# Kernel optimization log

Hardware: AMD Instinct MI355X
Metric: run time of the kernel (lower is better)

## Reference

```python
import jax, jax.numpy as jnp
import numpy as np

NUM_HEADS = 8
EPS = 1e-12  # torch F.normalize default eps


def conv1x1(x, w):
    # x: [b,c,h,w], w: [o,c]
    return jnp.einsum('bchw,oc->bohw', x, w)


def dwconv3x3(x, w):
    # depthwise 3x3, w: [c,1,3,3]
    return jax.lax.conv_general_dilated(
        x, w, window_strides=(1, 1), padding=((1, 1), (1, 1)),
        dimension_numbers=('NCHW', 'OIHW', 'NCHW'),
        feature_group_count=x.shape[1])


def l2norm(x):
    n = jnp.sqrt(jnp.sum(x * x, axis=-1, keepdims=True))
    return x / jnp.maximum(n, EPS)


def channel_attn(q, k, v, temperature, b, c, h, w):
    hd = c // NUM_HEADS
    q = l2norm(q.reshape(b, NUM_HEADS, hd, h * w))
    k = l2norm(k.reshape(b, NUM_HEADS, hd, h * w))
    v = v.reshape(b, NUM_HEADS, hd, h * w)
    attn = jnp.einsum('bndl,bnel->bnde', q, k) * temperature  # [b,nh,hd,hd]
    attn = jax.nn.softmax(attn, axis=-1)
    out = jnp.einsum('bnde,bnel->bndl', attn, v)
    return out.reshape(b, c, h, w)


def fdfp(x, w1, w2, h, w):
    xf = jnp.fft.rfft2(x, norm='ortho')  # over last two axes
    xfreq = jnp.concatenate([xf.real, xf.imag], axis=1)
    xfreq = conv1x1(xfreq, w1)
    xfreq = jax.nn.gelu(xfreq, approximate=False)
    xfreq = conv1x1(xfreq, w2)
    c2 = xfreq.shape[1] // 2
    xc = jax.lax.complex(xfreq[:, :c2], xfreq[:, c2:])
    return jnp.fft.irfft2(xc, s=(h, w), norm='ortho')


def setup_inputs() -> dict:
    key = jax.random.key(0)
    ks = jax.random.split(key, 10)
    dim = 192
    b, h, w = 4, 128, 128
    s = 0.05
    return {
        'x': jax.random.normal(ks[0], (b, dim, h, w), jnp.float32),
        'w_qkv1': jax.random.normal(ks[1], (3 * dim, dim), jnp.float32) * s,
        'w_qkv1_dw': jax.random.normal(ks[2], (3 * dim, 1, 3, 3), jnp.float32) * s,
        'w_proj1': jax.random.normal(ks[3], (dim, dim), jnp.float32) * s,
        'w_fdfp1': jax.random.normal(ks[4], (2 * dim, 2 * dim), jnp.float32) * s,
        'w_fdfp2': jax.random.normal(ks[5], (2 * dim, 2 * dim), jnp.float32) * s,
        'w_kv2': jax.random.normal(ks[6], (2 * dim, dim), jnp.float32) * s,
        'w_kv2_dw': jax.random.normal(ks[7], (2 * dim, 1, 3, 3), jnp.float32) * s,
        'w_proj2': jax.random.normal(ks[8], (dim, dim), jnp.float32) * s,
        'temperature': jnp.ones((NUM_HEADS, 1, 1), jnp.float32),
    }


def reference(x, w_qkv1, w_qkv1_dw, w_proj1, w_fdfp1, w_fdfp2,
              w_kv2, w_kv2_dw, w_proj2, temperature):
    b, c, h, w = x.shape
    # Stage 1: spatial-domain transposed (channel) attention
    qkv1 = dwconv3x3(conv1x1(x, w_qkv1), w_qkv1_dw)
    q1, k1, v1 = jnp.split(qkv1, 3, axis=1)
    out1 = channel_attn(q1, k1, v1, temperature, b, c, h, w)
    out1 = conv1x1(out1, w_proj1)
    # Stage 2: frequency-domain query, spatial K/V from stage-1 output
    q2 = fdfp(x, w_fdfp1, w_fdfp2, h, w)
    kv2 = dwconv3x3(conv1x1(out1, w_kv2), w_kv2_dw)
    k2, v2 = jnp.split(kv2, 2, axis=1)
    out2 = channel_attn(q2, k2, v2, temperature, b, c, h, w)
    out2 = conv1x1(out2, w_proj2)
    return out2
```

## Files before the change

kernel.cpp:

```cpp
#include <hip/hip_runtime.h>
#include <math.h>

typedef _Float16 half_t;
typedef half_t h8v __attribute__((ext_vector_type(8)));
typedef half_t h4v __attribute__((ext_vector_type(4)));
typedef float f32x4 __attribute__((ext_vector_type(4)));

namespace {
constexpr int DIMC = 192;
constexpr int NB = 4;
constexpr int HH = 128, WW = 128;
constexpr int HW = HH * WW;
constexpr int NH = 8, HD = 24;
constexpr int FP = 80;
constexpr long LT_PART = 128L * 192 * FP;
constexpr long LT_B    = 2 * LT_PART;
constexpr long LT_ROW  = 192L * FP;
constexpr long XB  = 192L * HW;
constexpr long CB0 = 0;
constexpr long CB1 = 15728640;
constexpr long OFF_T1 = 37748736;
constexpr long OFF_Q2 = 50331648;
constexpr long OFF_S  = 62914560;
constexpr long OFF_KT = 0;
constexpr long OFF_KF = 25165824;
constexpr long OFF_O2 = 0;
constexpr int  GSL = 64;
constexpr long SM_INVQ1 = OFF_S;
constexpr long SM_INVK1 = OFF_S + 768;
constexpr long SM_INVQ2 = OFF_S + 1536;
constexpr long SM_INVK2 = OFF_S + 2304;
constexpr long SM_ATT   = OFF_S + 3072;
constexpr long H0       = OFF_S + 168960;
constexpr long H_WQKV = H0;
constexpr long H_WF   = H0 + 55296;
constexpr long H_W1   = H0 + 92160;
constexpr long H_W2   = H0 + 165888;
constexpr long H_PRJ  = H0 + 239616;
constexpr long H_B2   = H0 + 258048;
constexpr long H_B3   = H0 + 290816;
constexpr long H_B1T  = H0 + 323584;
constexpr long H_B4T  = H0 + 333824;
constexpr float PI2 = 6.283185307179586476f;
}

__global__ void cvt16_k(const float* __restrict__ in, half_t* __restrict__ o, int n) {
    int i = blockIdx.x * 256 + threadIdx.x;
    if (i < n) o[i] = (half_t)in[i];
}
__global__ void initB1t_k(half_t* __restrict__ B) {
    int idx = blockIdx.x * 256 + threadIdx.x;
    if (idx >= 160 * 128) return;
    int j = idx / 128, k = idx % 128;
    float v = 0.f;
    if (j < 65) v = cosf(PI2 * ((k * j) & 127) / 128.f) * (1.f / 128.f);
    else if (j >= 80 && j < 145) v = -sinf(PI2 * ((k * (j - 80)) & 127) / 128.f) * (1.f / 128.f);
    B[idx] = (half_t)v;
}
__global__ void initB2h_k(half_t* __restrict__ B) {
    int idx = blockIdx.x * 256 + threadIdx.x;
    int m = idx >> 8, cin = idx & 255;
    int pd = m >> 7, ky = m & 127;
    int ps = cin >> 7, y = cin & 127;
    float c, s; sincosf(PI2 * ((ky * y) & 127) / 128.f, &s, &c);
    float v = (pd == 0) ? (ps == 0 ? c : s) : (ps == 0 ? -s : c);
    B[idx] = (half_t)v;
}
__global__ void initB3h_k(half_t* __restrict__ B) {
    int idx = blockIdx.x * 256 + threadIdx.x;
    int m = idx >> 8, cin = idx & 255;
    int pd = m >> 7, y = m & 127;
    int ps = cin >> 7, ky = cin & 127;
    float c, s; sincosf(PI2 * ((y * ky) & 127) / 128.f, &s, &c);
    float v = (pd == 0) ? (ps == 0 ? c : -s) : (ps == 0 ? s : c);
    B[idx] = (half_t)v;
}
__global__ void initB4t_k(half_t* __restrict__ B) {
    int idx = blockIdx.x * 256 + threadIdx.x;
    if (idx >= 128 * 160) return;
    int j = idx / 160, k = idx % 160;
    float v = 0.f;
    if (k < 80) {
        if (k == 0) v = 1.f / 128.f;
        else if (k < 64) v = 2.f * cosf(PI2 * ((k * j) & 127) / 128.f) / 128.f;
        else if (k == 64) v = cosf(PI2 * ((64 * j) & 127) / 128.f) / 128.f;
    } else {
        int kx = k - 80;
        if (kx >= 1 && kx < 64) v = -2.f * sinf(PI2 * ((kx * j) & 127) / 128.f) / 128.f;
    }
    B[idx] = (half_t)v;
}
__global__ void fusew_k(const float* __restrict__ wkv, const float* __restrict__ wproj,
                        half_t* __restrict__ wf) {
    int o = blockIdx.x, c = threadIdx.x;
    float acc = 0.f;
    for (int m = 0; m < 192; ++m) acc += wkv[o * 192 + m] * wproj[m * 192 + c];
    wf[o * 192 + c] = (half_t)acc;
}

template<int NW>
__global__ __launch_bounds__(NW * 64) void kcv(
    const half_t* __restrict__ W, const float* __restrict__ X, long xB,
    float* __restrict__ out, long oB) {
    __shared__ __align__(16) half_t S[6 * 64 * 40];
    const int t = threadIdx.x;
    const long p0 = (long)blockIdx.x * 64;
    const long xb = (long)blockIdx.y * xB;
    const long ob = (long)blockIdx.y * oB;
    const int lane = t & 63, wv = t >> 6;
    const int fr = lane & 15, fg = lane >> 4;
    {
        const int sp = t & 63;
        const int g = t >> 6;
        const float* gp = X + xb + p0 + sp;
        for (int grp = g; grp < 48; grp += NW) {
            int ci0 = grp * 4;
            h4v h;
#pragma unroll
            for (int j = 0; j < 4; ++j) h[j] = (half_t)gp[(long)(ci0 + j) * HW];
            *(h4v*)&S[((ci0 >> 5) * 64 + sp) * 40 + (ci0 & 31)] = h;
        }
    }
    __syncthreads();
    f32x4 acc[3][4];
#pragma unroll
    for (int m = 0; m < 3; ++m)
#pragma unroll
        for (int n = 0; n < 4; ++n) acc[m][n] = {0.f, 0.f, 0.f, 0.f};
    for (int k0 = 0; k0 < 192; k0 += 32) {
        const int s = k0 >> 5;
        h8v a[3], bb[4];
#pragma unroll
        for (int m = 0; m < 3; ++m)
            a[m] = *(const h8v*)(W + (long)(wv * 48 + m * 16 + fr) * 192 + k0 + fg * 8);
#pragma unroll
        for (int n = 0; n < 4; ++n)
            bb[n] = *(const h8v*)&S[(s * 64 + n * 16 + fr) * 40 + fg * 8];
#pragma unroll
        for (int m = 0; m < 3; ++m)
#pragma unroll
            for (int n = 0; n < 4; ++n)
                acc[m][n] = __builtin_amdgcn_mfma_f32_16x16x32_f16(a[m], bb[n], acc[m][n], 0, 0, 0);
    }
#pragma unroll
    for (int m = 0; m < 3; ++m)
#pragma unroll
        for (int i = 0; i < 4; ++i) {
            int o = wv * 48 + m * 16 + fg * 4 + i;
            float* row = out + ob + (long)o * HW + p0;
#pragma unroll
            for (int n = 0; n < 4; ++n) row[n * 16 + fr] = acc[m][n][i];
        }
}

template<int IN16, int OUT16>
__global__ __launch_bounds__(256) void k2big(
    const half_t* __restrict__ B16,
    const void* __restrict__ Xv, void* __restrict__ outv) {
    __shared__ __align__(16) half_t Xh[8 * 64 * 40];
    const int t = threadIdx.x;
    const long p0 = (long)blockIdx.x * 64;
    const long xb = (long)blockIdx.y * LT_B;
    const int lane = t & 63, wv = t >> 6;
    const int fr = lane & 15, fg = lane >> 4;
    {
        const int sp = t & 63;
        const int c0 = t >> 6;
#pragma unroll 8
        for (int j = 0; j < 64; ++j) {
            int ci = c0 + j * 4;
            long rb = (ci < 128) ? (long)ci * LT_ROW : (long)(ci - 128) * LT_ROW + LT_PART;
            half_t hv;
            if (IN16) hv = ((const half_t*)Xv)[xb + p0 + sp + rb];
            else      hv = (half_t)((const float*)Xv)[xb + p0 + sp + rb];
            Xh[((ci >> 5) * 64 + sp) * 40 + (ci & 31)] = hv;
        }
    }
    __syncthreads();
    f32x4 acc[4][4];
#pragma unroll
    for (int m = 0; m < 4; ++m)
#pragma unroll
        for (int n = 0; n < 4; ++n) acc[m][n] = {0.f, 0.f, 0.f, 0.f};
    for (int k0 = 0; k0 < 256; k0 += 32) {
        const int s = k0 >> 5;
        h8v a[4], bb[4];
#pragma unroll
        for (int m = 0; m < 4; ++m)
            a[m] = *(const h8v*)(B16 + (long)(wv * 64 + m * 16 + fr) * 256 + k0 + fg * 8);
#pragma unroll
        for (int n = 0; n < 4; ++n)
            bb[n] = *(const h8v*)&Xh[(s * 64 + n * 16 + fr) * 40 + fg * 8];
#pragma unroll
        for (int m = 0; m < 4; ++m)
#pragma unroll
            for (int n = 0; n < 4; ++n)
                acc[m][n] = __builtin_amdgcn_mfma_f32_16x16x32_f16(a[m], bb[n], acc[m][n], 0, 0, 0);
    }
#pragma unroll
    for (int m = 0; m < 4; ++m)
#pragma unroll
        for (int i = 0; i < 4; ++i) {
            int o = wv * 64 + m * 16 + fg * 4 + i;
            long oadr = xb + ((o < 128) ? (long)o * LT_ROW : (long)(o - 128) * LT_ROW + LT_PART);
#pragma unroll
            for (int n = 0; n < 4; ++n) {
                long idx = oadr + p0 + n * 16 + fr;
                if (OUT16) ((half_t*)outv)[idx] = (half_t)acc[m][n][i];
                else       ((float*)outv)[idx]  = acc[m][n][i];
            }
        }
}

__global__ __launch_bounds__(512) void kff4h(
    const half_t* __restrict__ W1, const half_t* __restrict__ W2,
    const half_t* __restrict__ X, half_t* __restrict__ out) {
    __shared__ __align__(16) half_t S[12 * 64 * 40];
    const int t = threadIdx.x;
    const long p0 = (long)blockIdx.x * 64;
    const long xb = (long)blockIdx.y * LT_B;
    const int lane = t & 63, wv = t >> 6;
    const int fr = lane & 15, fg = lane >> 4;
    {
        const int sp = t & 63;
        const int g = t >> 6;
        long pa; { long p = p0 + sp; long q = p / 80; pa = q * LT_ROW + (p - q * 80); }
        const half_t* gp = X + xb + pa;
#pragma unroll
        for (int ch = 0; ch < 12; ++ch) {
            int ci0 = ch * 32 + g * 4;
            h4v h;
#pragma unroll
            for (int j = 0; j < 4; ++j) {
                int ci = ci0 + j;
                long rb = (ci < 192) ? (long)ci * 80 : (long)(ci - 192) * 80 + LT_PART;
                h[j] = gp[rb];
            }
            *(h4v*)&S[(ch * 64 + sp) * 40 + g * 4] = h;
        }
    }
    __syncthreads();
    f32x4 acc[3][4];
#pragma unroll
    for (int m = 0; m < 3; ++m)
#pragma unroll
        for (int n = 0; n < 4; ++n) acc[m][n] = {0.f, 0.f, 0.f, 0.f};
    for (int k0 = 0; k0 < 384; k0 += 32) {
        const int s = k0 >> 5;
        h8v a[3], bb[4];
#pragma unroll
        for (int m = 0; m < 3; ++m)
            a[m] = *(const h8v*)(W1 + (long)(wv * 48 + m * 16 + fr) * 384 + k0 + fg * 8);
#pragma unroll
        for (int n = 0; n < 4; ++n)
            bb[n] = *(const h8v*)&S[(s * 64 + n * 16 + fr) * 40 + fg * 8];
#pragma unroll
        for (int m = 0; m < 3; ++m)
#pragma unroll
            for (int n = 0; n < 4; ++n)
                acc[m][n] = __builtin_amdgcn_mfma_f32_16x16x32_f16(a[m], bb[n], acc[m][n], 0, 0, 0);
    }
    __syncthreads();
#pragma unroll
    for (int m = 0; m < 3; ++m)
#pragma unroll
        for (int n = 0; n < 4; ++n) {
            int o4 = wv * 48 + m * 16 + fg * 4;
            int p = n * 16 + fr;
            h4v h;
#pragma unroll
            for (int i = 0; i < 4; ++i) {
                float v = acc[m][n][i];
                v = 0.5f * v * (1.f + erff(v * 0.70710678118654752f));
                h[i] = (half_t)v;
            }
            *(h4v*)&S[((o4 >> 5) * 64 + p) * 40 + (o4 & 31)] = h;
        }
#pragma unroll
    for (int m = 0; m < 3; ++m)
#pragma unroll
        for (int n = 0; n < 4; ++n) acc[m][n] = {0.f, 0.f, 0.f, 0.f};
    __syncthreads();
    for (int k0 = 0; k0 < 384; k0 += 32) {
        const int s = k0 >> 5;
        h8v a[3], bb[4];
#pragma unroll
        for (int m = 0; m < 3; ++m)
            a[m] = *(const h8v*)(W2 + (long)(wv * 48 + m * 16 + fr) * 384 + k0 + fg * 8);
#pragma unroll
        for (int n = 0; n < 4; ++n)
            bb[n] = *(const h8v*)&S[(s * 64 + n * 16 + fr) * 40 + fg * 8];
#pragma unroll
        for (int m = 0; m < 3; ++m)
#pragma unroll
            for (int n = 0; n < 4; ++n)
                acc[m][n] = __builtin_amdgcn_mfma_f32_16x16x32_f16(a[m], bb[n], acc[m][n], 0, 0, 0);
    }
    long pe[4];
#pragma unroll
    for (int n = 0; n < 4; ++n) {
        long p = p0 + n * 16 + fr;
        long q = p / 80; pe[n] = q * LT_ROW + (p - q * 80);
    }
#pragma unroll
    for (int m = 0; m < 3; ++m)
#pragma unroll
        for (int i = 0; i < 4; ++i) {
            int o = wv * 48 + m * 16 + fg * 4 + i;
            long oadr = xb + ((o < 192) ? (long)o * 80 : (long)(o - 192) * 80 + LT_PART);
#pragma unroll
            for (int n = 0; n < 4; ++n) out[oadr + pe[n]] = (half_t)acc[m][n][i];
        }
}

template<int NF, int NORM, int OUT16>
__global__ __launch_bounds__(256) void k1m(
    const float* __restrict__ A, long aBatch, long aC, long aRow, int aSplit, long aHiOff, int K,
    const uint* __restrict__ Bt32,
    void* __restrict__ outv, long oBatch, long oC, long oRow, int oSplit, long oHiOff,
    float* __restrict__ inv) {
    __shared__ __align__(16) half_t Ah[128 * 40];
    __shared__ __align__(16) half_t Bh[160 * 40];
    const int t = threadIdx.x;
    const long ab = (long)blockIdx.z * aBatch + (long)blockIdx.x * aC;
    const long ob = (long)blockIdx.z * oBatch + (long)blockIdx.x * oC;
    const int N = NF * 32;
    const int lane = t & 63, wv = t >> 6;
    const int wm = wv >> 1, wn = wv & 1;
    const int fr = lane & 15, fg = lane >> 4;
    const int sr = t >> 1, shalf = t & 1;
    const int Kw = K >> 1;
    f32x4 acc[4][NF];
#pragma unroll
    for (int m = 0; m < 4; ++m)
#pragma unroll
        for (int n = 0; n < NF; ++n) acc[m][n] = {0.f, 0.f, 0.f, 0.f};
    for (int k0 = 0; k0 < K; k0 += 32) {
        __syncthreads();
        {
            int cb = k0 + shalf * 16;
            long rb = (cb < aSplit) ? (long)cb : (long)(cb - aSplit) + aHiOff;
            const float* g = A + ab + (long)sr * aRow + rb;
            float4 v0 = *(const float4*)g;
            float4 v1 = *(const float4*)(g + 4);
            float4 v2 = *(const float4*)(g + 8);
            float4 v3 = *(const float4*)(g + 12);
            h8v h0, h1;
            h0[0] = (half_t)v0.x; h0[1] = (half_t)v0.y; h0[2] = (half_t)v0.z; h0[3] = (half_t)v0.w;
            h0[4] = (half_t)v1.x; h0[5] = (half_t)v1.y; h0[6] = (half_t)v1.z; h0[7] = (half_t)v1.w;
            h1[0] = (half_t)v2.x; h1[1] = (half_t)v2.y; h1[2] = (half_t)v2.z; h1[3] = (half_t)v2.w;
            h1[4] = (half_t)v3.x; h1[5] = (half_t)v3.y; h1[6] = (half_t)v3.z; h1[7] = (half_t)v3.w;
            *(h8v*)&Ah[sr * 40 + shalf * 16] = h0;
            *(h8v*)&Ah[sr * 40 + shalf * 16 + 8] = h1;
        }
        for (int j = t; j < N * 16; j += 256) {
            int n = j >> 4, kw = j & 15;
            *(uint*)&Bh[n * 40 + kw * 2] = Bt32[(long)n * Kw + (k0 >> 1) + kw];
        }
        __syncthreads();
        h8v a[4], bb[NF];
#pragma unroll
        for (int m = 0; m < 4; ++m) a[m] = *(const h8v*)&Ah[(wm * 64 + m * 16 + fr) * 40 + fg * 8];
#pragma unroll
        for (int n = 0; n < NF; ++n) bb[n] = *(const h8v*)&Bh[(wn * NF * 16 + n * 16 + fr) * 40 + fg * 8];
#pragma unroll
        for (int m = 0; m < 4; ++m)
#pragma unroll
            for (int n = 0; n < NF; ++n)
                acc[m][n] = __builtin_amdgcn_mfma_f32_16x16x32_f16(a[m], bb[n], acc[m][n], 0, 0, 0);
    }
#pragma unroll
    for (int m = 0; m < 4; ++m)
#pragma unroll
        for (int i = 0; i < 4; ++i) {
            int r = wm * 64 + m * 16 + fg * 4 + i;
            long rbase = ob + (long)r * oRow;
#pragma unroll
            for (int n = 0; n < NF; ++n) {
                int j = wn * NF * 16 + n * 16 + fr;
                long jm = (j < oSplit) ? (long)j : (long)(j - oSplit) + oHiOff;
                if (OUT16) ((half_t*)outv)[rbase + jm] = (half_t)acc[m][n][i];
                else       ((float*)outv)[rbase + jm]  = acc[m][n][i];
            }
        }
    if (NORM) {
        float ss = 0.f;
#pragma unroll
        for (int m = 0; m < 4; ++m)
#pragma unroll
            for (int n = 0; n < NF; ++n)
#pragma unroll
                for (int i = 0; i < 4; ++i) ss += acc[m][n][i] * acc[m][n][i];
        __syncthreads();
        float* red = (float*)Ah;
        red[t] = ss;
        __syncthreads();
        for (int st = 128; st > 0; st >>= 1) {
            if (t < st) red[t] += red[t + st];
            __syncthreads();
        }
        if (t == 0) inv[(long)blockIdx.z * 192 + blockIdx.x] = 1.f / fmaxf(sqrtf(red[0]), 1e-12f);
    }
}

__global__ __launch_bounds__(256) void dw3_k(
    const float* __restrict__ in, long inBatch,
    const float* __restrict__ w9,
    float* __restrict__ out, long outBatch,
    int normCnt, float* __restrict__ inv) {
    const int c = blockIdx.x, b = blockIdx.y;
    const int t = threadIdx.x;
    const float* ip = in + (long)b * inBatch + (long)c * HW;
    float* op = out + (long)b * outBatch + (long)c * HW;
    const float* wp = w9 + c * 9;
    const float w0 = wp[0], w1 = wp[1], w2 = wp[2];
    const float w3 = wp[3], w4 = wp[4], w5 = wp[5];
    const float w6 = wp[6], w7 = wp[7], w8 = wp[8];
    const int tx = t & 31;
    const int x0 = tx * 4;
    const int y0 = (t >> 5) * 16;
    const bool lx = (tx > 0), rx = (tx < 31);
    float Ar[6], Br[6], Cr[6];
#define LOADROW(Y, R) do { \
        const float* _p = ip + (Y) * 128 + x0; \
        float4 _v = *(const float4*)_p; \
        R[1] = _v.x; R[2] = _v.y; R[3] = _v.z; R[4] = _v.w; \
        R[0] = lx ? _p[-1] : 0.f; \
        R[5] = rx ? _p[4] : 0.f; } while (0)
    if (y0 == 0) { Ar[0]=Ar[1]=Ar[2]=Ar[3]=Ar[4]=Ar[5]=0.f; }
    else LOADROW(y0 - 1, Ar);
    LOADROW(y0, Br);
    float ss = 0.f;
#pragma unroll
    for (int i = 0; i < 16; ++i) {
        int y = y0 + i;
        if (y + 1 < 128) { LOADROW(y + 1, Cr); }
        else { Cr[0]=Cr[1]=Cr[2]=Cr[3]=Cr[4]=Cr[5]=0.f; }
        float o0 = Ar[0]*w0 + Ar[1]*w1 + Ar[2]*w2
                 + Br[0]*w3 + Br[1]*w4 + Br[2]*w5
                 + Cr[0]*w6 + Cr[1]*w7 + Cr[2]*w8;
        float o1 = Ar[1]*w0 + Ar[2]*w1 + Ar[3]*w2
                 + Br[1]*w3 + Br[2]*w4 + Br[3]*w5
                 + Cr[1]*w6 + Cr[2]*w7 + Cr[3]*w8;
        float o2 = Ar[2]*w0 + Ar[3]*w1 + Ar[4]*w2
                 + Br[2]*w3 + Br[3]*w4 + Br[4]*w5
                 + Cr[2]*w6 + Cr[3]*w7 + Cr[4]*w8;
        float o3 = Ar[3]*w0 + Ar[4]*w1 + Ar[5]*w2
                 + Br[3]*w3 + Br[4]*w4 + Br[5]*w5
                 + Cr[3]*w6 + Cr[4]*w7 + Cr[5]*w8;
        *(float4*)(op + y * 128 + x0) = make_float4(o0, o1, o2, o3);
        ss += o0*o0 + o1*o1 + o2*o2 + o3*o3;
#pragma unroll
        for (int j = 0; j < 6; ++j) { Ar[j] = Br[j]; Br[j] = Cr[j]; }
    }
#undef LOADROW
    if (normCnt > 0 && c < normCnt) {
        __shared__ float red[256];
        red[t] = ss;
        __syncthreads();
        for (int st = 128; st > 0; st >>= 1) {
            if (t < st) red[t] += red[t + st];
            __syncthreads();
        }
        if (t == 0) inv[(long)b * 192 + c] = 1.f / fmaxf(sqrtf(red[0]), 1e-12f);
    }
}

__global__ __launch_bounds__(576) void gramf_k(
    const float* __restrict__ q, long qB,
    const float* __restrict__ k, long kB,
    float* __restrict__ gp) {
    __shared__ float qs[HD][260];
    __shared__ float ks[HD][260];
    const int bn = blockIdx.x, ls = blockIdx.y;
    const int b = bn >> 3, n = bn & 7;
    const int t = threadIdx.x;
    const int l0 = ls * 256;
    const float* qp = q + (long)b * qB + (long)(n * HD) * HW + l0;
    const float* kp = k + (long)b * kB + (long)(n * HD) * HW + l0;
    for (int idx = t; idx < HD * 64; idx += 576) {
        int row = idx >> 6, c4 = (idx & 63) * 4;
        *(float4*)&qs[row][c4] = *(const float4*)(qp + (long)row * HW + c4);
        *(float4*)&ks[row][c4] = *(const float4*)(kp + (long)row * HW + c4);
    }
    __syncthreads();
    const int d = t / 24, e = t - d * 24;
    float acc = 0.f;
#pragma unroll 8
    for (int j = 0; j < 256; j += 4) {
        float4 a = *(const float4*)&qs[d][j];
        float4 bb = *(const float4*)&ks[e][j];
        acc += a.x * bb.x + a.y * bb.y + a.z * bb.z + a.w * bb.w;
    }
    gp[((long)bn * 576 + t) * GSL + ls] = acc;
}

__global__ __launch_bounds__(256) void softmax_k(
    const float* __restrict__ gp, const float* __restrict__ invq,
    const float* __restrict__ invk, const float* __restrict__ temp,
    float* __restrict__ attn) {
    int bn = blockIdx.x;
    int b = bn >> 3, n = bn & 7;
    int t = threadIdx.x;
    __shared__ float sums[576];
    for (int idx = t; idx < 576; idx += 256) {
        const float* g = gp + ((long)bn * 576 + idx) * GSL;
        float s = 0.f;
        for (int i = 0; i < GSL; i += 4) {
            float4 v = *(const float4*)(g + i);
            s += v.x + v.y + v.z + v.w;
        }
        sums[idx] = s;
    }
    __syncthreads();
    int d = t;
    if (d >= HD) return;
    float tt = temp[n];
    float iq = invq[b * 192 + n * HD + d];
    float row[HD];
#pragma unroll
    for (int e = 0; e < HD; ++e)
        row[e] = sums[d * HD + e] * iq * invk[b * 192 + n * HD + e] * tt;
    float m = row[0];
#pragma unroll
    for (int e = 1; e < HD; ++e) m = fmaxf(m, row[e]);
    float ssum = 0.f;
#pragma unroll
    for (int e = 0; e < HD; ++e) { row[e] = expf(row[e] - m); ssum += row[e]; }
    float is = 1.f / ssum;
#pragma unroll
    for (int e = 0; e < HD; ++e) attn[(long)bn * 576 + d * HD + e] = row[e] * is;
}

__global__ void attnapply_k(const float* __restrict__ attn, const float* __restrict__ v,
                            long vB, float* __restrict__ out, long outB) {
    int p = blockIdx.x * 256 + threadIdx.x;
    int bn = blockIdx.y;
    int b = bn >> 3, n = bn & 7;
    __shared__ float a[576];
    for (int i = threadIdx.x; i < 576; i += 256) a[i] = attn[(long)bn * 576 + i];
    __syncthreads();
    const float* vp = v + (long)b * vB + (long)(n * HD) * HW + p;
    float acc[HD];
#pragma unroll
    for (int d = 0; d < HD; ++d) acc[d] = 0.f;
    for (int e = 0; e < HD; ++e) {
        float vv = vp[(long)e * HW];
#pragma unroll
        for (int d = 0; d < HD; ++d) acc[d] += a[d * HD + e] * vv;
    }
    float* op = out + (long)b * outB + (long)(n * HD) * HW + p;
#pragma unroll
    for (int d = 0; d < HD; ++d) op[(long)d * HW] = acc[d];
}

extern "C" void kernel_launch(void* const* d_in, const int* in_sizes, int n_in,
                              void* d_out, int out_size, void* d_ws, size_t ws_size,
                              hipStream_t stream) {
    const float* x        = (const float*)d_in[0];
    const float* w_qkv1   = (const float*)d_in[1];
    const float* w_qkv1dw = (const float*)d_in[2];
    const float* w_proj1  = (const float*)d_in[3];
    const float* w_fdfp1  = (const float*)d_in[4];
    const float* w_fdfp2  = (const float*)d_in[5];
    const float* w_kv2    = (const float*)d_in[6];
    const float* w_kv2dw  = (const float*)d_in[7];
    const float* w_proj2  = (const float*)d_in[8];
    const float* temp     = (const float*)d_in[9];
    float* out = (float*)d_out;
    float* ws  = (float*)d_ws;
    dim3 blk(256);
    const int BIG = 1 << 20;

    cvt16_k<<<432, blk, 0, stream>>>(w_qkv1, (half_t*)(ws + H_WQKV), 110592);
    cvt16_k<<<576, blk, 0, stream>>>(w_fdfp1, (half_t*)(ws + H_W1), 147456);
    cvt16_k<<<576, blk, 0, stream>>>(w_fdfp2, (half_t*)(ws + H_W2), 147456);
    cvt16_k<<<144, blk, 0, stream>>>(w_proj2, (half_t*)(ws + H_PRJ), 36864);
    initB1t_k<<<80, blk, 0, stream>>>((half_t*)(ws + H_B1T));
    initB2h_k<<<256, blk, 0, stream>>>((half_t*)(ws + H_B2));
    initB3h_k<<<256, blk, 0, stream>>>((half_t*)(ws + H_B3));
    initB4t_k<<<80, blk, 0, stream>>>((half_t*)(ws + H_B4T));
    fusew_k<<<384, 192, 0, stream>>>(w_kv2, w_proj1, (half_t*)(ws + H_WF));

    k1m<5, 0, 1><<<dim3(192, 1, 4), blk, 0, stream>>>(
        x, XB, (long)HW, 128L, BIG, 0L, 128,
        (const uint*)(ws + H_B1T),
        (void*)(ws + CB0), LT_B, (long)FP, LT_ROW, 80, LT_PART, nullptr);
    k2big<1, 1><<<dim3(240, 4), blk, 0, stream>>>(
        (const half_t*)(ws + H_B2), (const void*)(ws + CB0), (void*)(ws + CB1));
    kff4h<<<dim3(160, 4), 512, 0, stream>>>(
        (const half_t*)(ws + H_W1), (const half_t*)(ws + H_W2),
        (const half_t*)(ws + CB1), (half_t*)(ws + CB0));
    k2big<1, 0><<<dim3(240, 4), blk, 0, stream>>>(
        (const half_t*)(ws + H_B3), (const void*)(ws + CB0), (void*)(ws + CB1));
    k1m<4, 1, 0><<<dim3(192, 1, 4), blk, 0, stream>>>(
        ws + CB1, LT_B, (long)FP, LT_ROW, 80, LT_PART, 160,
        (const uint*)(ws + H_B4T),
        (void*)(ws + OFF_Q2), XB, (long)HW, 128L, BIG, 0L, ws + SM_INVQ2);

    for (int ch = 0; ch < 3; ++ch) {
        kcv<4><<<dim3(256, 4), 256, 0, stream>>>(
            (const half_t*)(ws + H_WQKV) + (long)ch * 192 * 192,
            x, XB, ws + OFF_T1, XB);
        dw3_k<<<dim3(192, 4), blk, 0, stream>>>(
            ws + OFF_T1, XB, w_qkv1dw + ch * 192 * 9,
            ws + (long)ch * 192 * HW, (long)576 * HW,
            ch == 2 ? 0 : 192,
            ch == 0 ? ws + SM_INVQ1 : ws + SM_INVK1);
    }
    gramf_k<<<dim3(32, GSL), 576, 0, stream>>>(
        ws, (long)576 * HW, ws + (long)192 * HW, (long)576 * HW, ws + OFF_T1);
    softmax_k<<<32, blk, 0, stream>>>(ws + OFF_T1, ws + SM_INVQ1, ws + SM_INVK1, temp, ws + SM_ATT);
    attnapply_k<<<dim3(64, 32), blk, 0, stream>>>(
        ws + SM_ATT, ws + (long)384 * HW, (long)576 * HW, ws + OFF_T1, XB);

    kcv<8><<<dim3(256, 4), 512, 0, stream>>>(
        (const half_t*)(ws + H_WF), ws + OFF_T1, XB, ws + OFF_KT, (long)384 * HW);
    dw3_k<<<dim3(384, 4), blk, 0, stream>>>(
        ws + OFF_KT, (long)384 * HW, w_kv2dw, ws + OFF_KF, (long)384 * HW,
        192, ws + SM_INVK2);

    gramf_k<<<dim3(32, GSL), 576, 0, stream>>>(
        ws + OFF_Q2, XB, ws + OFF_KF, (long)384 * HW, ws + OFF_KT);
    softmax_k<<<32, blk, 0, stream>>>(ws + OFF_KT, ws + SM_INVQ2, ws + SM_INVK2, temp, ws + SM_ATT);
    attnapply_k<<<dim3(64, 32), blk, 0, stream>>>(
        ws + SM_ATT, ws + OFF_KF + (long)192 * HW, (long)384 * HW, ws + OFF_O2, XB);
    kcv<4><<<dim3(256, 4), 256, 0, stream>>>(
        (const half_t*)(ws + H_PRJ), ws + OFF_O2, XB, out, XB);
}
```

Measured before the change: 580.7 us.

## Replace shared-memory staged DFT GEMM with direct global-to-register MFMA operand loads

The row-DFT GEMM kernels (k1m, renamed k1big) no longer stage A and B tiles through LDS with two barriers per k-step. Each wave now loads its own 32 rows of A straight from global memory, converting to fp16 in registers, and reads the full B fragments directly from global. K becomes a template parameter so the loop can be fully unrolled. This removes LDS traffic and synchronisation, but every wave re-reads the whole B matrix from global/L2 and issues more uncoalesced loads.

```diff
diff --git a/kernel.cpp b/kernel.cpp
--- a/kernel.cpp
+++ b/kernel.cpp
@@ -313,71 +313,56 @@
         }
 }
 
-template<int NF, int NORM, int OUT16>
-__global__ __launch_bounds__(256) void k1m(
-    const float* __restrict__ A, long aBatch, long aC, long aRow, int aSplit, long aHiOff, int K,
-    const uint* __restrict__ Bt32,
+template<int NF, int NORM, int OUT16, int K>
+__global__ __launch_bounds__(256) void k1big(
+    const float* __restrict__ A, long aBatch, long aC, long aRow, int aSplit, long aHiOff,
+    const half_t* __restrict__ Bt,
     void* __restrict__ outv, long oBatch, long oC, long oRow, int oSplit, long oHiOff,
     float* __restrict__ inv) {
-    __shared__ __align__(16) half_t Ah[128 * 40];
-    __shared__ __align__(16) half_t Bh[160 * 40];
     const int t = threadIdx.x;
-    const long ab = (long)blockIdx.z * aBatch + (long)blockIdx.x * aC;
-    const long ob = (long)blockIdx.z * oBatch + (long)blockIdx.x * oC;
-    const int N = NF * 32;
+    const long ab = (long)blockIdx.y * aBatch + (long)blockIdx.x * aC;
+    const long ob = (long)blockIdx.y * oBatch + (long)blockIdx.x * oC;
     const int lane = t & 63, wv = t >> 6;
-    const int wm = wv >> 1, wn = wv & 1;
     const int fr = lane & 15, fg = lane >> 4;
-    const int sr = t >> 1, shalf = t & 1;
-    const int Kw = K >> 1;
-    f32x4 acc[4][NF];
-#pragma unroll
-    for (int m = 0; m < 4; ++m)
-#pragma unroll
-        for (int n = 0; n < NF; ++n) acc[m][n] = {0.f, 0.f, 0.f, 0.f};
+    constexpr int NFR = NF * 2;
+    f32x4 acc[2][NFR];
+#pragma unroll
+    for (int m = 0; m < 2; ++m)
+#pragma unroll
+        for (int n = 0; n < NFR; ++n) acc[m][n] = {0.f, 0.f, 0.f, 0.f};
     for (int k0 = 0; k0 < K; k0 += 32) {
-        __syncthreads();
-        {
-            int cb = k0 + shalf * 16;
-            long rb = (cb < aSplit) ? (long)cb : (long)(cb - aSplit) + aHiOff;
-            const float* g = A + ab + (long)sr * aRow + rb;
+        int kk = k0 + fg * 8;
+        long ka = (kk < aSplit) ? (long)kk : (long)(kk - aSplit) + aHiOff;
+        h8v a[2];
+#pragma unroll
+        for (int m = 0; m < 2; ++m) {
+            const float* g = A + ab + (long)(wv * 32 + m * 16 + fr) * aRow + ka;
             float4 v0 = *(const float4*)g;
             float4 v1 = *(const float4*)(g + 4);
-            float4 v2 = *(const float4*)(g + 8);
-            float4 v3 = *(const float4*)(g + 12);
-            h8v h0, h1;
-            h0[0] = (half_t)v0.x; h0[1] = (half_t)v0.y; h0[2] = (half_t)v0.z; h0[3] = (half_t)v0.w;
-            h0[4] = (half_t)v1.x; h0[5] = (half_t)v1.y; h0[6] = (half_t)v1.z; h0[7] = (half_t)v1.w;
-            h1[0] = (half_t)v2.x; h1[1] = (half_t)v2.y; h1[2] = (half_t)v2.z; h1[3] = (half_t)v2.w;
-            h1[4] = (half_t)v3.x; h1[5] = (half_t)v3.y; h1[6] = (half_t)v3.z; h1[7] = (half_t)v3.w;
-            *(h8v*)&Ah[sr * 40 + shalf * 16] = h0;
-            *(h8v*)&Ah[sr * 40 + shalf * 16 + 8] = h1;
-        }
-        for (int j = t; j < N * 16; j += 256) {
-            int n = j >> 4, kw = j & 15;
-            *(uint*)&Bh[n * 40 + kw * 2] = Bt32[(long)n * Kw + (k0 >> 1) + kw];
-        }
-        __syncthreads();
-        h8v a[4], bb[NF];
-#pragma unroll
-        for (int m = 0; m < 4; ++m) a[m] = *(const h8v*)&Ah[(wm * 64 + m * 16 + fr) * 40 + fg * 8];
-#pragma unroll
-        for (int n = 0; n < NF; ++n) bb[n] = *(const h8v*)&Bh[(wn * NF * 16 + n * 16 + fr) * 40 + fg * 8];
-#pragma unroll
-        for (int m = 0; m < 4; ++m)
-#pragma unroll
-            for (int n = 0; n < NF; ++n)
+            a[m][0] = (half_t)v0.x; a[m][1] = (half_t)v0.y;
+            a[m][2] = (half_t)v0.z; a[m][3] = (half_t)v0.w;
+            a[m][4] = (half_t)v1.x; a[m][5] = (half_t)v1.y;
+            a[m][6] = (half_t)v1.z; a[m][7] = (half_t)v1.w;
+        }
+        h8v bb[NFR];
+#pragma unroll
+        for (int n = 0; n < NFR; ++n)
+            bb[n] = *(const h8v*)(Bt + (long)(n * 16 + fr) * K + kk);
+#pragma unroll
+        for (int m = 0; m < 2; ++m)
+#pragma unroll
+            for (int n = 0; n < NFR; ++n)
                 acc[m][n] = __builtin_amdgcn_mfma_f32_16x16x32_f16(a[m], bb[n], acc[m][n], 0, 0, 0);
     }
 #pragma unroll
-    for (int m = 0; m < 4; ++m)
+    for (int m = 0; m < 2; ++m)
 #pragma unroll
         for (int i = 0; i < 4; ++i) {
-            int r = wm * 64 + m * 16 + fg * 4 + i;
+            int r = wv * 32 + m * 16 + fg * 4 + i;
             long rbase = ob + (long)r * oRow;
 #pragma unroll
-            for (int n = 0; n < NF; ++n) {
-                int j = wn * NF * 16 + n * 16 + fr;
+            for (int n = 0; n < NFR; ++n) {
+                int j = n * 16 + fr;
                 long jm = (j < oSplit) ? (long)j : (long)(j - oSplit) + oHiOff;
                 if (OUT16) ((half_t*)outv)[rbase + jm] = (half_t)acc[m][n][i];
                 else       ((float*)outv)[rbase + jm]  = acc[m][n][i];
@@ -386,20 +371,19 @@
     if (NORM) {
         float ss = 0.f;
 #pragma unroll
-        for (int m = 0; m < 4; ++m)
-#pragma unroll
-            for (int n = 0; n < NF; ++n)
+        for (int m = 0; m < 2; ++m)
+#pragma unroll
+            for (int n = 0; n < NFR; ++n)
 #pragma unroll
                 for (int i = 0; i < 4; ++i) ss += acc[m][n][i] * acc[m][n][i];
-        __syncthreads();
-        float* red = (float*)Ah;
+        __shared__ float red[256];
         red[t] = ss;
         __syncthreads();
         for (int st = 128; st > 0; st >>= 1) {
             if (t < st) red[t] += red[t + st];
             __syncthreads();
         }
-        if (t == 0) inv[(long)blockIdx.z * 192 + blockIdx.x] = 1.f / fmaxf(sqrtf(red[0]), 1e-12f);
+        if (t == 0) inv[(long)blockIdx.y * 192 + blockIdx.x] = 1.f / fmaxf(sqrtf(red[0]), 1e-12f);
     }
 }
 
@@ -582,9 +566,9 @@
     initB4t_k<<<80, blk, 0, stream>>>((half_t*)(ws + H_B4T));
     fusew_k<<<384, 192, 0, stream>>>(w_kv2, w_proj1, (half_t*)(ws + H_WF));
 
-    k1m<5, 0, 1><<<dim3(192, 1, 4), blk, 0, stream>>>(
-        x, XB, (long)HW, 128L, BIG, 0L, 128,
-        (const uint*)(ws + H_B1T),
+    k1big<5, 0, 1, 128><<<dim3(192, 4), blk, 0, stream>>>(
+        x, XB, (long)HW, 128L, BIG, 0L,
+        (const half_t*)(ws + H_B1T),
         (void*)(ws + CB0), LT_B, (long)FP, LT_ROW, 80, LT_PART, nullptr);
     k2big<1, 1><<<dim3(240, 4), blk, 0, stream>>>(
         (const half_t*)(ws + H_B2), (const void*)(ws + CB0), (void*)(ws + CB1));
@@ -593,9 +577,9 @@
         (const half_t*)(ws + CB1), (half_t*)(ws + CB0));
     k2big<1, 0><<<dim3(240, 4), blk, 0, stream>>>(
         (const half_t*)(ws + H_B3), (const void*)(ws + CB0), (void*)(ws + CB1));
-    k1m<4, 1, 0><<<dim3(192, 1, 4), blk, 0, stream>>>(
-        ws + CB1, LT_B, (long)FP, LT_ROW, 80, LT_PART, 160,
-        (const uint*)(ws + H_B4T),
+    k1big<4, 1, 0, 160><<<dim3(192, 4), blk, 0, stream>>>(
+        ws + CB1, LT_B, (long)FP, LT_ROW, 80, LT_PART,
+        (const half_t*)(ws + H_B4T),
         (void*)(ws + OFF_Q2), XB, (long)HW, 128L, BIG, 0L, ws + SM_INVQ2);
 
     for (int ch = 0; ch < 3; ++ch) {
```

New measurement: 578.4 us. About the same (-0.4%).
